# Kernel optimization log

Measured on AMD Instinct MI355X. Metric: run time of the kernel, lower is better.

## Reference

```python
import jax, jax.numpy as jnp
import numpy as np

B, S, D, H = 8, 1024, 1024, 16
DH = D // H  # 64
SCALE = (DH // H) ** (-0.5)  # faithful to torch: (key.size(-1) // num_heads) ** -0.5 = 4**-0.5 = 0.5
LN_EPS = 1e-5


def setup_inputs() -> dict:
    key = jax.random.key(0)
    ks = jax.random.split(key, 12)
    f = jnp.float32
    return {
        "key":   jax.random.normal(ks[0], (B, S, D), f),
        "value": jax.random.normal(ks[1], (B, S, D), f),
        "query": jax.random.normal(ks[2], (B, S, D), f),
        "Wq": jax.random.normal(ks[3], (D, D), f) * 0.02,
        "bq": jnp.zeros((D,), f),
        "Wk": jax.random.normal(ks[4], (D, D), f) * 0.02,
        "bk": jnp.zeros((D,), f),
        "Wv": jax.random.normal(ks[5], (D, D), f) * 0.02,
        "bv": jnp.zeros((D,), f),
        "Wo": jax.random.normal(ks[6], (D, D), f) * 0.02,
        "bo": jnp.zeros((D,), f),
        "ln_gamma": jnp.ones((D,), f),
        "ln_beta": jnp.zeros((D,), f),
    }


def _layer_norm(x, gamma, beta):
    mu = jnp.mean(x, axis=-1, keepdims=True)
    var = jnp.mean(jnp.square(x - mu), axis=-1, keepdims=True)
    return (x - mu) * jax.lax.rsqrt(var + LN_EPS) * gamma + beta


def reference(key, value, query, Wq, bq, Wk, bk, Wv, bv, Wo, bo, ln_gamma, ln_beta):
    residual = query
    # QKV projections (torch Linear: x @ W.T + b)
    k = key @ Wk.T + bk
    v = value @ Wv.T + bv
    q = query @ Wq.T + bq
    # Faithful raw view [B,S,H*dh] -> [B*H, S, dh] (row-major reshape, as in torch .view)
    k = k.reshape(B * H, S, DH)
    v = v.reshape(B * H, S, DH)
    q = q.reshape(B * H, S, DH)
    # scores: [B*H, S, S], softmax over last axis (dim=2)
    attn = jnp.einsum("bid,bjd->bij", q, k) * SCALE
    attn = jax.nn.softmax(attn, axis=2)
    context = jnp.einsum("bij,bjd->bid", attn, v)
    context = context.reshape(B, S, D)  # faithful raw view back
    out = context @ Wo.T + bo
    out = _layer_norm(residual + out, ln_gamma, ln_beta)
    return out, attn
```

## Files before the change

### kernel.cpp

```cpp
#include <hip/hip_runtime.h>
#include <stdint.h>

typedef unsigned short ushort_t;
typedef __attribute__((ext_vector_type(8))) short s16x8;
typedef __attribute__((ext_vector_type(8))) unsigned short u16x8;
typedef __attribute__((ext_vector_type(4))) unsigned short u16x4;
typedef __attribute__((ext_vector_type(4))) float f32x4;

#define AS1C(p) ((const __attribute__((address_space(1))) void*)(p))
#define AS3(p)  ((__attribute__((address_space(3))) void*)(p))

#define QSCALE 0.7213475204444817f

#define EXP2F(x) __builtin_amdgcn_exp2f(x)
#define LOG2F(x) __builtin_amdgcn_logf(x)

#define WAVE_LDS_FENCE()                                    \
  do {                                                      \
    asm volatile("s_waitcnt lgkmcnt(0)" ::: "memory");      \
    __builtin_amdgcn_sched_barrier(0);                      \
  } while (0)

#define SBAR()                                              \
  do {                                                      \
    __builtin_amdgcn_sched_barrier(0);                      \
    __builtin_amdgcn_s_barrier();                           \
    __builtin_amdgcn_sched_barrier(0);                      \
  } while (0)

__device__ __forceinline__ ushort_t f2bf(float f) {
  uint32_t u = __float_as_uint(f);
  u += 0x7fffu + ((u >> 16) & 1u);
  return (ushort_t)(u >> 16);
}
__device__ __forceinline__ float bf2f(ushort_t h) {
  return __uint_as_float(((uint32_t)h) << 16);
}

__global__ __launch_bounds__(256) void cvt3_kernel(const float* __restrict__ s0,
                                                   const float* __restrict__ s1,
                                                   const float* __restrict__ s2,
                                                   ushort_t* __restrict__ dst) {
  const int y = blockIdx.y;
  const float* src = y == 0 ? s0 : (y == 1 ? s1 : s2);
  const int i = blockIdx.x * 256 + threadIdx.x;
  const float4 v = ((const float4*)src)[i];
  ushort4 o;
  o.x = f2bf(v.x); o.y = f2bf(v.y); o.z = f2bf(v.z); o.w = f2bf(v.w);
  ((ushort4*)(dst + (size_t)y * 8388608))[i] = o;
}

__global__ __launch_bounds__(256) void cvtw_kernel(const float* __restrict__ w0,
                                                   const float* __restrict__ w1,
                                                   const float* __restrict__ w2,
                                                   const float* __restrict__ w3,
                                                   ushort_t* __restrict__ dqkv,
                                                   ushort_t* __restrict__ dwo) {
  const int y = blockIdx.y;
  const float* src = y == 0 ? w0 : (y == 1 ? w1 : (y == 2 ? w2 : w3));
  ushort_t* dst = y < 3 ? dqkv + (size_t)y * 1048576 : dwo;
  const float sc = y == 0 ? QSCALE : 1.0f;
  const int i = blockIdx.x * 256 + threadIdx.x;
  const float4 v = ((const float4*)src)[i];
  ushort4 o;
  o.x = f2bf(v.x * sc); o.y = f2bf(v.y * sc); o.z = f2bf(v.z * sc); o.w = f2bf(v.w * sc);
  ((ushort4*)dst)[i] = o;
}

__global__ __launch_bounds__(256) void biascat_kernel(const float* __restrict__ bq,
                                                      const float* __restrict__ bk,
                                                      const float* __restrict__ bv,
                                                      float* __restrict__ dst) {
  const int i = blockIdx.x * 256 + threadIdx.x;
  dst[i] = i < 1024 ? bq[i] * QSCALE : (i < 2048 ? bk[i - 1024] : bv[i - 2048]);
}

template <int OUT_BF16>
__global__ __launch_bounds__(512) void gemm_nt(const ushort_t* __restrict__ A0,
                                               const ushort_t* __restrict__ A1,
                                               const ushort_t* __restrict__ A2,
                                               const ushort_t* __restrict__ B,
                                               const float* __restrict__ bias,
                                               void* __restrict__ C0,
                                               void* __restrict__ C1,
                                               void* __restrict__ C2) {
  __shared__ ushort_t As[3][128 * 32];
  __shared__ ushort_t Bs[3][128 * 32];
  const int tid = threadIdx.x;
  const int w = tid >> 6, lane = tid & 63, g = lane >> 4, c = lane & 15;
  const int wm = w >> 1, wn = w & 1;
  const int m0 = blockIdx.y * 128, n0 = blockIdx.x * 128;
  const int sel = n0 >> 10, nloc0 = n0 & 1023;
  const ushort_t* A = sel == 0 ? A0 : (sel == 1 ? A1 : A2);
  char* C = (char*)(sel == 0 ? C0 : (sel == 1 ? C1 : C2));
  f32x4 acc[2][4] = {};

  const int srow = tid >> 2, scol = (tid & 3) << 3;
  const int sdst = (w * 64) * 8;

#define G_STAGE(buf, k0_)                                                                  \
  do {                                                                                     \
    __builtin_amdgcn_global_load_lds(AS1C(&A[(size_t)(m0 + srow) * 1024 + (k0_) + scol]),  \
                                     AS3(&As[buf][sdst]), 16, 0, 0);                       \
    __builtin_amdgcn_global_load_lds(AS1C(&B[(size_t)(n0 + srow) * 1024 + (k0_) + scol]),  \
                                     AS3(&Bs[buf][sdst]), 16, 0, 0);                       \
  } while (0)

  G_STAGE(0, 0);
  G_STAGE(1, 32);
  asm volatile("s_waitcnt vmcnt(2)" ::: "memory");
  SBAR();
  int cur = 0;
  for (int it = 0; it < 32; ++it) {
    if (it < 30) {
      const int sb = cur >= 1 ? cur - 1 : 2;
      G_STAGE(sb, 32 * (it + 2));
    }
    s16x8 af[2], bfr[4];
#pragma unroll
    for (int mi = 0; mi < 2; ++mi)
      af[mi] = *(const s16x8*)&As[cur][(wm * 32 + mi * 16 + c) * 32 + g * 8];
#pragma unroll
    for (int ni = 0; ni < 4; ++ni)
      bfr[ni] = *(const s16x8*)&Bs[cur][(wn * 64 + ni * 16 + c) * 32 + g * 8];
    __builtin_amdgcn_s_setprio(1);
#pragma unroll
    for (int mi = 0; mi < 2; ++mi)
#pragma unroll
      for (int ni = 0; ni < 4; ++ni)
        acc[mi][ni] = __builtin_amdgcn_mfma_f32_16x16x32_bf16(af[mi], bfr[ni], acc[mi][ni], 0, 0, 0);
    __builtin_amdgcn_s_setprio(0);
    if (it < 31) {
      if (it < 30)
        asm volatile("s_waitcnt vmcnt(2) lgkmcnt(0)" ::: "memory");
      else
        asm volatile("s_waitcnt vmcnt(0) lgkmcnt(0)" ::: "memory");
      SBAR();
    }
    cur = cur < 2 ? cur + 1 : 0;
  }
#undef G_STAGE

#pragma unroll
  for (int ni = 0; ni < 4; ++ni) {
    const int nn = wn * 64 + ni * 16 + c;
    const float bv = bias[n0 + nn];
#pragma unroll
    for (int mi = 0; mi < 2; ++mi) {
#pragma unroll
      for (int rr = 0; rr < 4; ++rr) {
        const int m = m0 + wm * 32 + mi * 16 + g * 4 + rr;
        const float val = acc[mi][ni][rr] + bv;
        if (OUT_BF16)
          ((ushort_t*)C)[(size_t)m * 1024 + nloc0 + nn] = f2bf(val);
        else
          ((float*)C)[(size_t)m * 1024 + nloc0 + nn] = val;
      }
    }
  }
}

__global__ __launch_bounds__(256) void transpose_v(const ushort_t* __restrict__ v,
                                                   ushort_t* __restrict__ vt) {
  __shared__ ushort_t T[64][72];
  const int n = blockIdx.y, ib = blockIdx.x;
  const int t = threadIdx.x;
  {
    const int row = t >> 2, cb = (t & 3) << 4;
    const ushort_t* src = v + (size_t)n * 65536 + (size_t)(ib * 64 + row) * 64 + cb;
    *(u16x8*)&T[row][cb] = *(const u16x8*)src;
    *(u16x8*)&T[row][cb + 8] = *(const u16x8*)(src + 8);
  }
  __syncthreads();
  {
    const int dh = t >> 2, ibs = (t & 3) << 4;
    u16x8 a, b;
#pragma unroll
    for (int e = 0; e < 8; ++e) { a[e] = T[ibs + e][dh]; b[e] = T[ibs + 8 + e][dh]; }
    ushort_t* dst = vt + (size_t)n * 65536 + (size_t)dh * 1024 + ib * 64 + ibs;
    *(u16x8*)dst = a;
    *(u16x8*)(dst + 8) = b;
  }
}

__global__ __launch_bounds__(256) void stats_kernel(const ushort_t* __restrict__ q,
                                                    const ushort_t* __restrict__ k,
                                                    float* __restrict__ bias_out) {
  __shared__ ushort_t Kb[3][64 * 64];
  const int wg = blockIdx.x;
  const int idx = ((wg & 7) << 7) | (wg >> 3);
  const int n = idx >> 3, qb = idx & 7;
  const int tid = threadIdx.x, w = tid >> 6, lane = tid & 63, g = lane >> 4, c = lane & 15;
  const int q0 = qb * 128 + w * 32;
  const ushort_t* qh = q + (size_t)n * 65536;
  const char* khb = (const char*)(k + (size_t)n * 65536);

  const int r0 = w * 16 + (lane >> 3);
  const int csw = (((lane & 7) ^ (lane >> 3)) << 4);

#define STAGE_KS(buf, jt_)                                                                  \
  do {                                                                                      \
    __builtin_amdgcn_global_load_lds(AS1C(khb + ((size_t)(jt_)*64 + r0) * 128 + csw),       \
                                     AS3(&Kb[buf][(w * 2 + 0) * 512]), 16, 0, 0);           \
    __builtin_amdgcn_global_load_lds(AS1C(khb + ((size_t)(jt_)*64 + r0 + 8) * 128 + csw),   \
                                     AS3(&Kb[buf][(w * 2 + 1) * 512]), 16, 0, 0);           \
  } while (0)
#define KFRAGS(buf, jn, h)                                                    \
  (*(const s16x8*)((const char*)&Kb[buf][0] +                                 \
                   (((((jn)*16 + c) * 128 + (h)*64 + g * 16)) ^ ((c & 7) << 4))))

  s16x8 aq[2][2];
#pragma unroll
  for (int fr = 0; fr < 2; ++fr) {
    aq[fr][0] = *(const s16x8*)&qh[(q0 + fr * 16 + c) * 64 + g * 8];
    aq[fr][1] = *(const s16x8*)&qh[(q0 + fr * 16 + c) * 64 + 32 + g * 8];
  }

  float l_acc[2][4] = {};

  STAGE_KS(0, 0);
  STAGE_KS(1, 1);
  asm volatile("s_waitcnt vmcnt(2)" ::: "memory");
  SBAR();
  int cur = 0;
  for (int jt = 0; jt < 16; ++jt) {
    if (jt < 14) {
      const int sb = cur >= 1 ? cur - 1 : 2;
      STAGE_KS(sb, jt + 2);
    }
    f32x4 sfr[2][4];
    __builtin_amdgcn_s_setprio(1);
#pragma unroll
    for (int fr = 0; fr < 2; ++fr)
#pragma unroll
      for (int jn = 0; jn < 4; ++jn) {
        f32x4 z = {0.f, 0.f, 0.f, 0.f};
        z = __builtin_amdgcn_mfma_f32_16x16x32_bf16(aq[fr][0], KFRAGS(cur, jn, 0), z, 0, 0, 0);
        z = __builtin_amdgcn_mfma_f32_16x16x32_bf16(aq[fr][1], KFRAGS(cur, jn, 1), z, 0, 0, 0);
        sfr[fr][jn] = z;
      }
    __builtin_amdgcn_s_setprio(0);
#pragma unroll
    for (int fr = 0; fr < 2; ++fr)
#pragma unroll
      for (int rr = 0; rr < 4; ++rr)
        l_acc[fr][rr] += EXP2F(sfr[fr][0][rr]) + EXP2F(sfr[fr][1][rr]) +
                         EXP2F(sfr[fr][2][rr]) + EXP2F(sfr[fr][3][rr]);
    if (jt < 15) {
      if (jt < 14)
        asm volatile("s_waitcnt vmcnt(2) lgkmcnt(0)" ::: "memory");
      else
        asm volatile("s_waitcnt vmcnt(0) lgkmcnt(0)" ::: "memory");
      SBAR();
    }
    cur = cur < 2 ? cur + 1 : 0;
  }

#pragma unroll
  for (int fr = 0; fr < 2; ++fr)
#pragma unroll
    for (int rr = 0; rr < 4; ++rr) {
      float l = l_acc[fr][rr];
      l += __shfl_xor(l, 1);
      l += __shfl_xor(l, 2);
      l += __shfl_xor(l, 4);
      l += __shfl_xor(l, 8);
      if (c == 0)
        bias_out[(size_t)n * 1024 + q0 + fr * 16 + g * 4 + rr] = LOG2F(l);
    }
#undef STAGE_KS
#undef KFRAGS
}

__global__ __launch_bounds__(256) void attn_kernel(const ushort_t* __restrict__ q,
                                                   const ushort_t* __restrict__ k,
                                                   const ushort_t* __restrict__ vt,
                                                   const float* __restrict__ stats,
                                                   float* __restrict__ attn,
                                                   ushort_t* __restrict__ ctx) {
  __shared__ ushort_t Kb[2][64 * 64];
  __shared__ ushort_t Vb[2][64 * 64];
  __shared__ ushort_t Pb[4][16 * 64];
  const int wg = blockIdx.x;
  const int idx = ((wg & 7) << 8) | (wg >> 3);
  const int n = idx >> 4, qb = idx & 15;
  const int tid = threadIdx.x, w = tid >> 6, lane = tid & 63, g = lane >> 4, c = lane & 15;
  const int i0 = qb * 64 + w * 16;
  const ushort_t* qh = q + (size_t)n * 65536;
  const char* khb = (const char*)(k + (size_t)n * 65536);
  const char* vhb = (const char*)(vt + (size_t)n * 65536);
  char* pwb = (char*)&Pb[w][0];

  const int r0 = w * 16 + (lane >> 3);
  const int csw = (((lane & 7) ^ (lane >> 3)) << 4);

#define STAGE_K(buf, jt_)                                                                   \
  do {                                                                                      \
    __builtin_amdgcn_global_load_lds(AS1C(khb + ((size_t)(jt_)*64 + r0) * 128 + csw),       \
                                     AS3(&Kb[buf][(w * 2 + 0) * 512]), 16, 0, 0);           \
    __builtin_amdgcn_global_load_lds(AS1C(khb + ((size_t)(jt_)*64 + r0 + 8) * 128 + csw),   \
                                     AS3(&Kb[buf][(w * 2 + 1) * 512]), 16, 0, 0);           \
  } while (0)
#define STAGE_V(buf, jt_)                                                                   \
  do {                                                                                      \
    __builtin_amdgcn_global_load_lds(AS1C(vhb + (size_t)r0 * 2048 + (jt_)*128 + csw),       \
                                     AS3(&Vb[buf][(w * 2 + 0) * 512]), 16, 0, 0);           \
    __builtin_amdgcn_global_load_lds(AS1C(vhb + (size_t)(r0 + 8) * 2048 + (jt_)*128 + csw), \
                                     AS3(&Vb[buf][(w * 2 + 1) * 512]), 16, 0, 0);           \
  } while (0)
#define KFRAG(buf, jn, h)                                                     \
  (*(const s16x8*)((const char*)&Kb[buf][0] +                                 \
                   (((((jn)*16 + c) * 128 + (h)*64 + g * 16)) ^ ((c & 7) << 4))))
#define VFRAG(buf, dn, ks_)                                                   \
  (*(const s16x8*)((const char*)&Vb[buf][0] +                                 \
                   (((((dn)*16 + c) * 128 + (ks_)*64 + g * 16)) ^ ((c & 7) << 4))))

  const s16x8 aq0 = *(const s16x8*)&qh[(i0 + c) * 64 + g * 8];
  const s16x8 aq1 = *(const s16x8*)&qh[(i0 + c) * 64 + 32 + g * 8];

  float bias_r[4];
  {
    const float* sb = stats + (size_t)n * 1024 + i0;
#pragma unroll
    for (int r = 0; r < 4; ++r) bias_r[r] = sb[4 * g + r];
  }

  f32x4 cacc[4] = {};
  float* arow = attn + (size_t)n * 1048576;

  STAGE_K(0, 0);
  STAGE_V(0, 0);
  asm volatile("s_waitcnt vmcnt(0) lgkmcnt(0)" ::: "memory");
  SBAR();
  for (int jt = 0; jt < 16; ++jt) {
    const int cur = jt & 1;
    if (jt < 15) { STAGE_K(cur ^ 1, jt + 1); STAGE_V(cur ^ 1, jt + 1); }
    f32x4 s[4];
    __builtin_amdgcn_s_setprio(1);
#pragma unroll
    for (int jn = 0; jn < 4; ++jn) {
      f32x4 z = {0.f, 0.f, 0.f, 0.f};
      z = __builtin_amdgcn_mfma_f32_16x16x32_bf16(aq0, KFRAG(cur, jn, 0), z, 0, 0, 0);
      z = __builtin_amdgcn_mfma_f32_16x16x32_bf16(aq1, KFRAG(cur, jn, 1), z, 0, 0, 0);
      s[jn] = z;
    }
    __builtin_amdgcn_s_setprio(0);
#pragma unroll
    for (int jn = 0; jn < 4; ++jn) {
#pragma unroll
      for (int r = 0; r < 4; ++r) {
        const float p = EXP2F(s[jn][r] - bias_r[r]);
        const int row = 4 * g + r;
        const int A = (row << 7) + ((jn * 16 + c) << 1);
        *(ushort_t*)(pwb + (A ^ ((row & 7) << 4))) = f2bf(p);
      }
    }
    WAVE_LDS_FENCE();
    __builtin_amdgcn_s_setprio(1);
#pragma unroll
    for (int ks = 0; ks < 2; ++ks) {
      const int A = (c << 7) + (ks << 6) + (g << 4);
      const s16x8 pa = *(const s16x8*)(pwb + (A ^ ((c & 7) << 4)));
#pragma unroll
      for (int dn = 0; dn < 4; ++dn)
        cacc[dn] = __builtin_amdgcn_mfma_f32_16x16x32_bf16(pa, VFRAG(cur, dn, ks), cacc[dn], 0, 0, 0);
    }
    __builtin_amdgcn_s_setprio(0);
#pragma unroll
    for (int e = 0; e < 4; ++e) {
      const int row = g + 4 * e;
      const int A = (row << 7) + (c << 3);
      const u16x4 hv = *(const u16x4*)(pwb + (A ^ ((row & 7) << 4)));
      f32x4 fv;
#pragma unroll
      for (int t2 = 0; t2 < 4; ++t2) fv[t2] = bf2f(hv[t2]);
      *(f32x4*)&arow[(size_t)(i0 + row) * 1024 + jt * 64 + c * 4] = fv;
    }
    if (jt < 15) {
      asm volatile("s_waitcnt vmcnt(4) lgkmcnt(0)" ::: "memory");
      SBAR();
    }
  }

  ushort_t* ch = ctx + (size_t)n * 65536;
#pragma unroll
  for (int dn = 0; dn < 4; ++dn)
#pragma unroll
    for (int r = 0; r < 4; ++r)
      ch[(size_t)(i0 + 4 * g + r) * 64 + dn * 16 + c] = f2bf(cacc[dn][r]);
#undef STAGE_K
#undef STAGE_V
#undef KFRAG
#undef VFRAG
}

__global__ __launch_bounds__(256) void ln_kernel(const float* __restrict__ proj,
                                                 const float* __restrict__ resid,
                                                 const float* __restrict__ gamma,
                                                 const float* __restrict__ beta,
                                                 float* __restrict__ out) {
  __shared__ float sred[4], ssred[4];
  const int row = blockIdx.x, t = threadIdx.x;
  const float4 pv = ((const float4*)(proj + (size_t)row * 1024))[t];
  const float4 rv = ((const float4*)(resid + (size_t)row * 1024))[t];
  float4 x;
  x.x = pv.x + rv.x; x.y = pv.y + rv.y; x.z = pv.z + rv.z; x.w = pv.w + rv.w;
  float s = x.x + x.y + x.z + x.w;
  float ss = x.x * x.x + x.y * x.y + x.z * x.z + x.w * x.w;
#pragma unroll
  for (int msk = 1; msk < 64; msk <<= 1) {
    s += __shfl_xor(s, msk);
    ss += __shfl_xor(ss, msk);
  }
  const int w = t >> 6, lane = t & 63;
  if (lane == 0) { sred[w] = s; ssred[w] = ss; }
  __syncthreads();
  s = sred[0] + sred[1] + sred[2] + sred[3];
  ss = ssred[0] + ssred[1] + ssred[2] + ssred[3];
  const float mu = s * (1.f / 1024.f);
  const float var = ss * (1.f / 1024.f) - mu * mu;
  const float rs = rsqrtf(var + 1e-5f);
  const float4 gm = ((const float4*)gamma)[t];
  const float4 bt = ((const float4*)beta)[t];
  float4 o;
  o.x = (x.x - mu) * rs * gm.x + bt.x;
  o.y = (x.y - mu) * rs * gm.y + bt.y;
  o.z = (x.z - mu) * rs * gm.z + bt.z;
  o.w = (x.w - mu) * rs * gm.w + bt.w;
  ((float4*)(out + (size_t)row * 1024))[t] = o;
}

extern "C" void kernel_launch(void* const* d_in, const int* in_sizes, int n_in,
                              void* d_out, int out_size, void* d_ws, size_t ws_size,
                              hipStream_t stream) {
  const float* key   = (const float*)d_in[0];
  const float* value = (const float*)d_in[1];
  const float* query = (const float*)d_in[2];
  const float* Wq = (const float*)d_in[3];  const float* bq = (const float*)d_in[4];
  const float* Wk = (const float*)d_in[5];  const float* bk = (const float*)d_in[6];
  const float* Wv = (const float*)d_in[7];  const float* bv = (const float*)d_in[8];
  const float* Wo = (const float*)d_in[9];  const float* bo = (const float*)d_in[10];
  const float* gamma = (const float*)d_in[11];
  const float* beta  = (const float*)d_in[12];

  char* ws = (char*)d_ws;
  ushort_t* q_   = (ushort_t*)(ws + 0);
  ushort_t* k_   = (ushort_t*)(ws + 16777216);
  ushort_t* vt_  = (ushort_t*)(ws + 33554432);
  ushort_t* ctx_ = (ushort_t*)(ws + 50331648);
  ushort_t* wo_  = (ushort_t*)(ws + 67108864);
  float*    proj_ = (float*)(ws + 0);

  char* o8 = (char*)d_out;
  float*    outp  = (float*)o8;
  float*    attnp = (float*)(o8 + 33554432);
  float*    stats = (float*)o8;
  ushort_t* xq   = (ushort_t*)(o8 + 33554432);
  ushort_t* xk   = (ushort_t*)(o8 + 50331648);
  ushort_t* xv   = (ushort_t*)(o8 + 67108864);
  ushort_t* wqkv = (ushort_t*)(o8 + 83886080);
  ushort_t* v_   = (ushort_t*)(o8 + 90177536);
  float*    bqkv = (float*)(o8 + 106954752);

  cvt3_kernel<<<dim3(8192, 3), 256, 0, stream>>>(query, key, value, xq);
  cvtw_kernel<<<dim3(1024, 4), 256, 0, stream>>>(Wq, Wk, Wv, Wo, wqkv, wo_);
  biascat_kernel<<<12, 256, 0, stream>>>(bq, bk, bv, bqkv);

  gemm_nt<1><<<dim3(24, 64), 512, 0, stream>>>(xq, xk, xv, wqkv, bqkv, q_, k_, v_);

  transpose_v<<<dim3(16, 128), 256, 0, stream>>>(v_, vt_);

  stats_kernel<<<1024, 256, 0, stream>>>(q_, k_, stats);

  attn_kernel<<<2048, 256, 0, stream>>>(q_, k_, vt_, stats, attnp, ctx_);

  gemm_nt<0><<<dim3(8, 64), 512, 0, stream>>>(ctx_, ctx_, ctx_, wo_, bo, proj_, proj_, proj_);

  ln_kernel<<<8192, 256, 0, stream>>>(proj_, query, gamma, beta, outp);
}
```

Measured before the change: 352.2 us.

## Process 32 query rows per wave in attention kernel and use nontemporal attn stores

```diff
diff --git a/kernel.cpp b/kernel.cpp
--- a/kernel.cpp
+++ b/kernel.cpp
@@ -280,12 +280,12 @@
                                                    ushort_t* __restrict__ ctx) {
   __shared__ ushort_t Kb[2][64 * 64];
   __shared__ ushort_t Vb[2][64 * 64];
-  __shared__ ushort_t Pb[4][16 * 64];
+  __shared__ ushort_t Pb[4][32 * 64];
   const int wg = blockIdx.x;
-  const int idx = ((wg & 7) << 8) | (wg >> 3);
-  const int n = idx >> 4, qb = idx & 15;
+  const int idx = ((wg & 7) << 7) | (wg >> 3);
+  const int n = idx >> 3, qb = idx & 7;
   const int tid = threadIdx.x, w = tid >> 6, lane = tid & 63, g = lane >> 4, c = lane & 15;
-  const int i0 = qb * 64 + w * 16;
+  const int i0 = qb * 128 + w * 32;
   const ushort_t* qh = q + (size_t)n * 65536;
   const char* khb = (const char*)(k + (size_t)n * 65536);
   const char* vhb = (const char*)(vt + (size_t)n * 65536);
@@ -315,17 +315,18 @@
   (*(const s16x8*)((const char*)&Vb[buf][0] +                                 \
                    (((((dn)*16 + c) * 128 + (ks_)*64 + g * 16)) ^ ((c & 7) << 4))))
 
-  const s16x8 aq0 = *(const s16x8*)&qh[(i0 + c) * 64 + g * 8];
-  const s16x8 aq1 = *(const s16x8*)&qh[(i0 + c) * 64 + 32 + g * 8];
-
-  float bias_r[4];
-  {
-    const float* sb = stats + (size_t)n * 1024 + i0;
-#pragma unroll
-    for (int r = 0; r < 4; ++r) bias_r[r] = sb[4 * g + r];
-  }
-
-  f32x4 cacc[4] = {};
+  s16x8 aq[2][2];
+  float bias_r[2][4];
+#pragma unroll
+  for (int fr = 0; fr < 2; ++fr) {
+    aq[fr][0] = *(const s16x8*)&qh[(i0 + fr * 16 + c) * 64 + g * 8];
+    aq[fr][1] = *(const s16x8*)&qh[(i0 + fr * 16 + c) * 64 + 32 + g * 8];
+    const float* sb = stats + (size_t)n * 1024 + i0 + fr * 16;
+#pragma unroll
+    for (int r = 0; r < 4; ++r) bias_r[fr][r] = sb[4 * g + r];
+  }
+
+  f32x4 cacc[2][4] = {};
   float* arow = attn + (size_t)n * 1048576;
 
   STAGE_K(0, 0);
@@ -335,59 +336,74 @@
   for (int jt = 0; jt < 16; ++jt) {
     const int cur = jt & 1;
     if (jt < 15) { STAGE_K(cur ^ 1, jt + 1); STAGE_V(cur ^ 1, jt + 1); }
-    f32x4 s[4];
+    f32x4 s[2][4];
     __builtin_amdgcn_s_setprio(1);
 #pragma unroll
-    for (int jn = 0; jn < 4; ++jn) {
-      f32x4 z = {0.f, 0.f, 0.f, 0.f};
-      z = __builtin_amdgcn_mfma_f32_16x16x32_bf16(aq0, KFRAG(cur, jn, 0), z, 0, 0, 0);
-      z = __builtin_amdgcn_mfma_f32_16x16x32_bf16(aq1, KFRAG(cur, jn, 1), z, 0, 0, 0);
-      s[jn] = z;
-    }
+    for (int fr = 0; fr < 2; ++fr)
+#pragma unroll
+      for (int jn = 0; jn < 4; ++jn) {
+        f32x4 z = {0.f, 0.f, 0.f, 0.f};
+        z = __builtin_amdgcn_mfma_f32_16x16x32_bf16(aq[fr][0], KFRAG(cur, jn, 0), z, 0, 0, 0);
+        z = __builtin_amdgcn_mfma_f32_16x16x32_bf16(aq[fr][1], KFRAG(cur, jn, 1), z, 0, 0, 0);
+        s[fr][jn] = z;
+      }
     __builtin_amdgcn_s_setprio(0);
 #pragma unroll
-    for (int jn = 0; jn < 4; ++jn) {
-#pragma unroll
-      for (int r = 0; r < 4; ++r) {
-        const float p = EXP2F(s[jn][r] - bias_r[r]);
-        const int row = 4 * g + r;
-        const int A = (row << 7) + ((jn * 16 + c) << 1);
-        *(ushort_t*)(pwb + (A ^ ((row & 7) << 4))) = f2bf(p);
-      }
-    }
+    for (int fr = 0; fr < 2; ++fr)
+#pragma unroll
+      for (int jn = 0; jn < 4; ++jn)
+#pragma unroll
+        for (int r = 0; r < 4; ++r) {
+          const float p = EXP2F(s[fr][jn][r] - bias_r[fr][r]);
+          const int row = fr * 16 + 4 * g + r;
+          const int A = (row << 7) + ((jn * 16 + c) << 1);
+          *(ushort_t*)(pwb + (A ^ ((row & 7) << 4))) = f2bf(p);
+        }
     WAVE_LDS_FENCE();
     __builtin_amdgcn_s_setprio(1);
 #pragma unroll
     for (int ks = 0; ks < 2; ++ks) {
-      const int A = (c << 7) + (ks << 6) + (g << 4);
-      const s16x8 pa = *(const s16x8*)(pwb + (A ^ ((c & 7) << 4)));
-#pragma unroll
-      for (int dn = 0; dn < 4; ++dn)
-        cacc[dn] = __builtin_amdgcn_mfma_f32_16x16x32_bf16(pa, VFRAG(cur, dn, ks), cacc[dn], 0, 0, 0);
+      s16x8 pa[2];
+#pragma unroll
+      for (int fr = 0; fr < 2; ++fr) {
+        const int A = ((fr * 16 + c) << 7) + (ks << 6) + (g << 4);
+        pa[fr] = *(const s16x8*)(pwb + (A ^ ((c & 7) << 4)));
+      }
+#pragma unroll
+      for (int dn = 0; dn < 4; ++dn) {
+        const s16x8 bv = VFRAG(cur, dn, ks);
+        cacc[0][dn] = __builtin_amdgcn_mfma_f32_16x16x32_bf16(pa[0], bv, cacc[0][dn], 0, 0, 0);
+        cacc[1][dn] = __builtin_amdgcn_mfma_f32_16x16x32_bf16(pa[1], bv, cacc[1][dn], 0, 0, 0);
+      }
     }
     __builtin_amdgcn_s_setprio(0);
 #pragma unroll
-    for (int e = 0; e < 4; ++e) {
-      const int row = g + 4 * e;
-      const int A = (row << 7) + (c << 3);
-      const u16x4 hv = *(const u16x4*)(pwb + (A ^ ((row & 7) << 4)));
-      f32x4 fv;
-#pragma unroll
-      for (int t2 = 0; t2 < 4; ++t2) fv[t2] = bf2f(hv[t2]);
-      *(f32x4*)&arow[(size_t)(i0 + row) * 1024 + jt * 64 + c * 4] = fv;
-    }
+    for (int fr = 0; fr < 2; ++fr)
+#pragma unroll
+      for (int e = 0; e < 4; ++e) {
+        const int row = fr * 16 + g + 4 * e;
+        const int A = (row << 7) + (c << 3);
+        const u16x4 hv = *(const u16x4*)(pwb + (A ^ ((row & 7) << 4)));
+        f32x4 fv;
+#pragma unroll
+        for (int t2 = 0; t2 < 4; ++t2) fv[t2] = bf2f(hv[t2]);
+        __builtin_nontemporal_store(
+            fv, (f32x4*)&arow[(size_t)(i0 + row) * 1024 + jt * 64 + c * 4]);
+      }
     if (jt < 15) {
-      asm volatile("s_waitcnt vmcnt(4) lgkmcnt(0)" ::: "memory");
+      asm volatile("s_waitcnt vmcnt(8) lgkmcnt(0)" ::: "memory");
       SBAR();
     }
   }
 
   ushort_t* ch = ctx + (size_t)n * 65536;
 #pragma unroll
-  for (int dn = 0; dn < 4; ++dn)
-#pragma unroll
-    for (int r = 0; r < 4; ++r)
-      ch[(size_t)(i0 + 4 * g + r) * 64 + dn * 16 + c] = f2bf(cacc[dn][r]);
+  for (int fr = 0; fr < 2; ++fr)
+#pragma unroll
+    for (int dn = 0; dn < 4; ++dn)
+#pragma unroll
+      for (int r = 0; r < 4; ++r)
+        ch[(size_t)(i0 + fr * 16 + 4 * g + r) * 64 + dn * 16 + c] = f2bf(cacc[fr][dn][r]);
 #undef STAGE_K
 #undef STAGE_V
 #undef KFRAG
@@ -472,7 +488,7 @@
 
   stats_kernel<<<1024, 256, 0, stream>>>(q_, k_, stats);
 
-  attn_kernel<<<2048, 256, 0, stream>>>(q_, k_, vt_, stats, attnp, ctx_);
+  attn_kernel<<<1024, 256, 0, stream>>>(q_, k_, vt_, stats, attnp, ctx_);
 
   gemm_nt<0><<<dim3(8, 64), 512, 0, stream>>>(ctx_, ctx_, ctx_, wo_, bo, proj_, proj_, proj_);
 
```

New measurement: 314.0 us, median of 2. 1.12x faster.
